# Kernel tuning notes

Hardware: AMD Instinct MI355X
Metric: run time of the kernel (lower is better)

The kernel has to match this reference:

```python
import jax, jax.numpy as jnp
import numpy as np

H, C, HID, L, NF, B = 4, 128, 128, 3, 5, 32  # heads, per-head dim, hidden, layers, node feats, graphs
LN_EPS = 1e-5


def setup_inputs() -> dict:
    key = jax.random.key(0)
    ks = jax.random.split(key, 12)
    N, E = 10000, 160000
    x = jax.random.normal(ks[0], (N, NF), dtype=jnp.float32)
    edge_index = jax.random.randint(ks[1], (2, E), 0, N, dtype=jnp.int64)
    batch = jnp.sort(jax.random.randint(ks[2], (N,), 0, B, dtype=jnp.int64))
    s = 0.1
    return {
        "x": x,
        "edge_index": edge_index,
        "batch": batch,
        "node_W": jax.random.normal(ks[3], (NF, HID), dtype=jnp.float32) * s,
        "node_b": jnp.zeros((HID,), dtype=jnp.float32),
        "Ws": jax.random.normal(ks[4], (L, HID, H * C), dtype=jnp.float32) * s,
        "att_srcs": jax.random.normal(ks[5], (L, H, C), dtype=jnp.float32) * s,
        "att_dsts": jax.random.normal(ks[6], (L, H, C), dtype=jnp.float32) * s,
        "biases": jnp.zeros((L, HID), dtype=jnp.float32),
        "ln_gs": jnp.ones((L, HID), dtype=jnp.float32),
        "ln_bs": jnp.zeros((L, HID), dtype=jnp.float32),
    }


def _layer_norm(x, g, b):
    mu = jnp.mean(x, axis=-1, keepdims=True)
    var = jnp.mean(jnp.square(x - mu), axis=-1, keepdims=True)
    return (x - mu) * jax.lax.rsqrt(var + LN_EPS) * g + b


def _gat_layer(x, W, att_src, att_dst, bias, src, dst, N):
    # x: [N, HID]; PyG GATConv, heads=H, concat=False (mean over heads)
    h = (x @ W).reshape(N, H, C)                       # [N,H,C]
    a_src = jnp.sum(h * att_src, axis=-1)              # [N,H]
    a_dst = jnp.sum(h * att_dst, axis=-1)              # [N,H]
    e = jax.nn.leaky_relu(a_src[src] + a_dst[dst], 0.2)  # [E,H]
    # edge-softmax over destination neighborhoods (numerically stable)
    m = jax.ops.segment_max(e, dst, num_segments=N)
    ex = jnp.exp(e - m[dst])
    denom = jax.ops.segment_sum(ex, dst, num_segments=N)
    alpha = ex / (denom[dst] + 1e-16)                  # [E,H]
    msg = h[src] * alpha[:, :, None]                   # [E,H,C]
    out = jax.ops.segment_sum(msg, dst, num_segments=N)  # [N,H,C]
    return out.mean(axis=1) + bias                     # concat=False -> head mean


def reference(x, edge_index, batch, node_W, node_b, Ws, att_srcs, att_dsts,
              biases, ln_gs, ln_bs):
    N = x.shape[0]
    loop = jnp.arange(N, dtype=edge_index.dtype)
    src = jnp.concatenate([edge_index[0], loop])       # PyG adds self-loops
    dst = jnp.concatenate([edge_index[1], loop])

    h = jax.nn.relu(x @ node_W + node_b)               # [N,HID]
    for l in range(L):
        h_new = _gat_layer(h, Ws[l], att_srcs[l], att_dsts[l], biases[l], src, dst, N)
        h_new = _layer_norm(h_new, ln_gs[l], ln_bs[l])
        h = jax.nn.relu(h_new) + h                     # residual; dropout is identity in eval

    # global mean pool over graphs
    sums = jax.ops.segment_sum(h, batch, num_segments=B)
    cnts = jax.ops.segment_sum(jnp.ones((N, 1), h.dtype), batch, num_segments=B)
    graph_emb = sums / jnp.maximum(cnts, 1.0)
    return h, graph_emb
```

## Files before the change

kernel.cpp:

```cpp
#include <hip/hip_runtime.h>
#include <math.h>

#define N_NODES 10000
#define N_EDGES 160000
#define E2 (N_EDGES + N_NODES)
#define HIDDEN 128
#define NHEAD 4
#define NB 32
#define LN_EPS 1e-5f

#define T_INPUT (N_NODES * HIDDEN)
#define T_HIST  (T_INPUT + N_EDGES)
#define T_CONV  (T_HIST + 3 * 512 * 128)
#define T_BOUND (T_CONV + N_NODES)
#define T_TOTAL T_BOUND

typedef __attribute__((ext_vector_type(8))) short bf16x8;
typedef __attribute__((ext_vector_type(4))) float f32x4;

__device__ __forceinline__ unsigned short f2bf(float f) {
    unsigned int u = __float_as_uint(f);
    u += 0x7fffu + ((u >> 16) & 1u);
    return (unsigned short)(u >> 16);
}
__device__ __forceinline__ float bf2f_lo(unsigned int u) { return __uint_as_float(u << 16); }
__device__ __forceinline__ float bf2f_hi(unsigned int u) { return __uint_as_float(u & 0xffff0000u); }

__global__ __launch_bounds__(256) void k_pre(const float* __restrict__ x,
                                             const float* __restrict__ W,
                                             const float* __restrict__ b,
                                             const int* __restrict__ ei,
                                             const int* __restrict__ batch,
                                             const float* __restrict__ Ws,
                                             float* __restrict__ h,
                                             unsigned short* __restrict__ hb,
                                             int* counts, int* gstart, int* gend,
                                             unsigned short* __restrict__ Btb) {
    int t = blockIdx.x * blockDim.x + threadIdx.x;
    if (t < T_INPUT) {
        int n = t >> 7, c = t & 127;
        float s = b[c];
        #pragma unroll
        for (int k = 0; k < 5; k++) s += x[n * 5 + k] * W[k * HIDDEN + c];
        float r = fmaxf(s, 0.f);
        h[t] = r;
        hb[t] = f2bf(r);
    } else if (t < T_HIST) {
        int e = t - T_INPUT;
        atomicAdd(&counts[ei[N_EDGES + e]], 1);
    } else if (t < T_CONV) {
        int i = t - T_HIST;
        int l = i >> 16, rem = i & 65535;
        int n = rem >> 7, k = rem & 127;
        Btb[i] = f2bf(Ws[l * 65536 + k * 512 + n]);
    } else if (t < T_BOUND) {
        int n = t - T_CONV;
        int bb = batch[n];
        if (n == 0 || batch[n - 1] != bb) gstart[bb] = n;
        if (n == N_NODES - 1 || batch[n + 1] != bb) gend[bb] = n + 1;
    }
}

__global__ void k_scan(const int* __restrict__ counts, int* rowptr, int* cursor) {
    __shared__ int sums[1024];
    int t = threadIdx.x;
    const int per = 10;
    int base = t * per;
    int loc[per];
    int s = 0;
    for (int i = 0; i < per; i++) {
        int idx = base + i;
        int v = (idx < N_NODES) ? counts[idx] + 1 : 0;
        loc[i] = s; s += v;
    }
    sums[t] = s;
    __syncthreads();
    for (int off = 1; off < 1024; off <<= 1) {
        int v = (t >= off) ? sums[t - off] : 0;
        __syncthreads();
        sums[t] += v;
        __syncthreads();
    }
    int prefix = (t > 0) ? sums[t - 1] : 0;
    for (int i = 0; i < per; i++) {
        int idx = base + i;
        if (idx < N_NODES) { int r = prefix + loc[i]; rowptr[idx] = r; cursor[idx] = r; }
    }
    if (t == 1023) rowptr[N_NODES] = sums[1023];
}

template <int SCATTER>
__global__ __launch_bounds__(256) void k_gemm_att(const unsigned short* __restrict__ Ab,
                                                  const unsigned short* __restrict__ Bt,
                                                  const float* __restrict__ ws,
                                                  const float* __restrict__ wd,
                                                  unsigned short* __restrict__ Cb,
                                                  float* __restrict__ a_src,
                                                  float* __restrict__ a_dst,
                                                  const int* __restrict__ ei,
                                                  int* __restrict__ cursor,
                                                  int* __restrict__ csr_src) {
    if (SCATTER) {
        int e = (blockIdx.y * gridDim.x + blockIdx.x) * 256 + threadIdx.x;
        if (e < N_EDGES) {
            int s = ei[e], d = ei[N_EDGES + e];
            int pos = atomicAdd(&cursor[d], 1);
            csr_src[pos] = s;
        } else if (e < E2) {
            int n = e - N_EDGES;
            int pos = atomicAdd(&cursor[n], 1);
            csr_src[pos] = n;
        }
    }
    int wave = threadIdx.x >> 6, lane = threadIdx.x & 63;
    int q = lane >> 4, u = lane & 15;
    int h = blockIdx.x;
    int rowgrp = wave & 1, colhalf = wave >> 1;
    int mbase = blockIdx.y * 32 + rowgrp * 16;
    int colbase = h * 128 + colhalf * 64;
    int arow = mbase + u;
    if (arow > N_NODES - 1) arow = N_NODES - 1;
    bf16x8 a[4];
    #pragma unroll
    for (int k0 = 0; k0 < 4; k0++)
        a[k0] = *(const bf16x8*)(Ab + (size_t)arow * 128 + k0 * 32 + q * 8);
    f32x4 acc[4];
    #pragma unroll
    for (int nb = 0; nb < 4; nb++) acc[nb] = (f32x4){0.f, 0.f, 0.f, 0.f};
    #pragma unroll
    for (int nb = 0; nb < 4; nb++) {
        const unsigned short* bp = Bt + (size_t)(colbase + nb * 16 + u) * 128 + q * 8;
        #pragma unroll
        for (int k0 = 0; k0 < 4; k0++) {
            bf16x8 bfr = *(const bf16x8*)(bp + k0 * 32);
            acc[nb] = __builtin_amdgcn_mfma_f32_16x16x32_bf16(a[k0], bfr, acc[nb], 0, 0, 0);
        }
    }
    #pragma unroll
    for (int nb = 0; nb < 4; nb++) {
        int col = colbase + nb * 16 + u;
        #pragma unroll
        for (int r = 0; r < 4; r++) {
            int row = mbase + q * 4 + r;
            if (row < N_NODES) Cb[(size_t)row * 512 + col] = f2bf(acc[nb][r]);
        }
    }
    float ps[4] = {}, pd[4] = {};
    #pragma unroll
    for (int nb = 0; nb < 4; nb++) {
        int cl = colhalf * 64 + nb * 16 + u;
        float wsv = ws[h * 128 + cl], wdv = wd[h * 128 + cl];
        #pragma unroll
        for (int r = 0; r < 4; r++) { ps[r] += acc[nb][r] * wsv; pd[r] += acc[nb][r] * wdv; }
    }
    #pragma unroll
    for (int d = 1; d < 16; d <<= 1) {
        #pragma unroll
        for (int r = 0; r < 4; r++) {
            ps[r] += __shfl_xor(ps[r], d);
            pd[r] += __shfl_xor(pd[r], d);
        }
    }
    __shared__ float ls[2][2][16], ldd[2][2][16];
    if (u == 0) {
        #pragma unroll
        for (int r = 0; r < 4; r++) {
            ls[rowgrp][colhalf][q * 4 + r] = ps[r];
            ldd[rowgrp][colhalf][q * 4 + r] = pd[r];
        }
    }
    __syncthreads();
    if (colhalf == 0 && lane < 16) {
        int row = mbase + lane;
        if (row < N_NODES) {
            a_src[row * 4 + h] = ls[rowgrp][0][lane] + ls[rowgrp][1][lane];
            a_dst[row * 4 + h] = ldd[rowgrp][0][lane] + ldd[rowgrp][1][lane];
        }
    }
}

__global__ __launch_bounds__(256) void k_agg(const uint4* __restrict__ hb4,
                                             const int* __restrict__ rowptr,
                                             const int* __restrict__ csr,
                                             const float* __restrict__ a_src,
                                             const float* __restrict__ a_dst,
                                             const float* __restrict__ bias,
                                             const float* __restrict__ lng,
                                             const float* __restrict__ lnb,
                                             float* __restrict__ h,
                                             unsigned short* __restrict__ hbn) {
    int wave = threadIdx.x >> 6;
    int lane = threadIdx.x & 63;
    int n = blockIdx.x * 4 + wave;
    if (n >= N_NODES) return;
    int hl = lane >> 4;
    int pos = lane & 15;
    int off = rowptr[n];
    int deg = rowptr[n + 1] - off;
    float adn = a_dst[n * 4 + hl];
    float mA = -INFINITY, dA = 0.f;
    float mB = -INFINITY, dB = 0.f;
    float oA[8] = {}, oB[8] = {};
    for (int base = 0; base < deg; base += 64) {
        int cnt = min(64, deg - base);
        int s = (lane < cnt) ? csr[off + base + lane] : 0;
        int i1 = (1 < cnt) ? 1 : 0;
        int s0 = __shfl(s, 0), s1 = __shfl(s, i1);
        uint4 u0 = hb4[(size_t)s0 * 64 + lane];
        float av0 = a_src[s0 * 4 + hl];
        uint4 u1 = hb4[(size_t)s1 * 64 + lane];
        float av1 = a_src[s1 * 4 + hl];
        for (int i = 0; i < cnt; i += 2) {
            int j2 = (i + 2 < cnt) ? i + 2 : cnt - 1;
            int j3 = (i + 3 < cnt) ? i + 3 : cnt - 1;
            int s2 = __shfl(s, j2), s3 = __shfl(s, j3);
            uint4 u2 = hb4[(size_t)s2 * 64 + lane];
            float av2 = a_src[s2 * 4 + hl];
            uint4 u3 = hb4[(size_t)s3 * 64 + lane];
            float av3 = a_src[s3 * 4 + hl];
            {
                float t = av0 + adn;
                float e = t > 0.f ? t : 0.2f * t;
                float nm = fmaxf(mA, e);
                float sc = __expf(mA - nm);
                float p = __expf(e - nm);
                dA = dA * sc + p;
                oA[0] = oA[0] * sc + p * bf2f_lo(u0.x);
                oA[1] = oA[1] * sc + p * bf2f_hi(u0.x);
                oA[2] = oA[2] * sc + p * bf2f_lo(u0.y);
                oA[3] = oA[3] * sc + p * bf2f_hi(u0.y);
                oA[4] = oA[4] * sc + p * bf2f_lo(u0.z);
                oA[5] = oA[5] * sc + p * bf2f_hi(u0.z);
                oA[6] = oA[6] * sc + p * bf2f_lo(u0.w);
                oA[7] = oA[7] * sc + p * bf2f_hi(u0.w);
                mA = nm;
            }
            if (i + 1 < cnt) {
                float t = av1 + adn;
                float e = t > 0.f ? t : 0.2f * t;
                float nm = fmaxf(mB, e);
                float sc = __expf(mB - nm);
                float p = __expf(e - nm);
                dB = dB * sc + p;
                oB[0] = oB[0] * sc + p * bf2f_lo(u1.x);
                oB[1] = oB[1] * sc + p * bf2f_hi(u1.x);
                oB[2] = oB[2] * sc + p * bf2f_lo(u1.y);
                oB[3] = oB[3] * sc + p * bf2f_hi(u1.y);
                oB[4] = oB[4] * sc + p * bf2f_lo(u1.z);
                oB[5] = oB[5] * sc + p * bf2f_hi(u1.z);
                oB[6] = oB[6] * sc + p * bf2f_lo(u1.w);
                oB[7] = oB[7] * sc + p * bf2f_hi(u1.w);
                mB = nm;
            }
            u0 = u2; av0 = av2;
            u1 = u3; av1 = av3;
        }
    }
    float M = fmaxf(mA, mB);
    float sA = __expf(mA - M);
    float sB = (mB == -INFINITY) ? 0.f : __expf(mB - M);
    float denom = dA * sA + dB * sB;
    float o[8];
    #pragma unroll
    for (int k = 0; k < 8; k++) o[k] = oA[k] * sA + oB[k] * sB;

    float inv = 1.f / (denom + 1e-16f);
    #pragma unroll
    for (int k = 0; k < 8; k++) o[k] *= inv;
    #pragma unroll
    for (int k = 0; k < 8; k++) {
        o[k] += __shfl_xor(o[k], 16);
        o[k] += __shfl_xor(o[k], 32);
    }
    float v[8], sv = 0.f, sq = 0.f;
    #pragma unroll
    for (int k = 0; k < 8; k++) {
        float b = bias[8 * pos + k];
        v[k] = 0.25f * o[k] + b;
        sv += v[k]; sq += v[k] * v[k];
    }
    #pragma unroll
    for (int d = 8; d > 0; d >>= 1) {
        sv += __shfl_xor(sv, d);
        sq += __shfl_xor(sq, d);
    }
    float mu = sv * (1.f / 128.f);
    float var = sq * (1.f / 128.f) - mu * mu;
    float rs = rsqrtf(var + LN_EPS);
    if (hl == 0) {
        float* hrow = h + (size_t)n * 128 + 8 * pos;
        float4 old0 = *(const float4*)(hrow);
        float4 old1 = *(const float4*)(hrow + 4);
        float r[8];
        #pragma unroll
        for (int k = 0; k < 8; k++) {
            float y = (v[k] - mu) * rs * lng[8 * pos + k] + lnb[8 * pos + k];
            r[k] = fmaxf(y, 0.f);
        }
        float w[8] = {r[0] + old0.x, r[1] + old0.y, r[2] + old0.z, r[3] + old0.w,
                      r[4] + old1.x, r[5] + old1.y, r[6] + old1.z, r[7] + old1.w};
        *(float4*)(hrow) = make_float4(w[0], w[1], w[2], w[3]);
        *(float4*)(hrow + 4) = make_float4(w[4], w[5], w[6], w[7]);
        ushort4 p0, p1;
        p0.x = f2bf(w[0]); p0.y = f2bf(w[1]); p0.z = f2bf(w[2]); p0.w = f2bf(w[3]);
        p1.x = f2bf(w[4]); p1.y = f2bf(w[5]); p1.z = f2bf(w[6]); p1.w = f2bf(w[7]);
        unsigned short* hbrow = hbn + (size_t)n * 128 + 8 * pos;
        *(ushort4*)(hbrow) = p0;
        *(ushort4*)(hbrow + 4) = p1;
    }
}

#define POOL_CHUNK 32
__global__ __launch_bounds__(128) void k_pool_sum(const float* __restrict__ h,
                                                  const int* __restrict__ batch,
                                                  const int* __restrict__ gstart,
                                                  const int* __restrict__ gend,
                                                  float* __restrict__ gout) {
    int n0 = blockIdx.x * POOL_CHUNK;
    int c = threadIdx.x;
    int nend = min(n0 + POOL_CHUNK, N_NODES);
    if (n0 >= N_NODES) return;
    int cur = batch[n0];
    float acc = 0.f;
    for (int n = n0; n < nend; n++) {
        int b = batch[n];
        if (b != cur) {
            float inv = 1.f / (float)max(gend[cur] - gstart[cur], 1);
            atomicAdd(&gout[cur * HIDDEN + c], acc * inv);
            acc = 0.f; cur = b;
        }
        acc += h[(size_t)n * HIDDEN + c];
    }
    float inv = 1.f / (float)max(gend[cur] - gstart[cur], 1);
    atomicAdd(&gout[cur * HIDDEN + c], acc * inv);
}

extern "C" void kernel_launch(void* const* d_in, const int* in_sizes, int n_in,
                              void* d_out, int out_size, void* d_ws, size_t ws_size,
                              hipStream_t stream) {
    const float* x      = (const float*)d_in[0];
    const int*   ei     = (const int*)d_in[1];
    const int*   batch  = (const int*)d_in[2];
    const float* node_W = (const float*)d_in[3];
    const float* node_b = (const float*)d_in[4];
    const float* Ws     = (const float*)d_in[5];
    const float* att_s  = (const float*)d_in[6];
    const float* att_d  = (const float*)d_in[7];
    const float* biases = (const float*)d_in[8];
    const float* ln_g   = (const float*)d_in[9];
    const float* ln_b   = (const float*)d_in[10];

    float* out = (float*)d_out;
    float* h = out;
    float* gout = out + (size_t)N_NODES * HIDDEN;

    char* w = (char*)d_ws;
    auto carve = [&](size_t bytes) {
        void* p = (void*)w;
        w += (bytes + 255) & ~(size_t)255;
        return p;
    };
    int* rowptr  = (int*)carve((N_NODES + 1) * sizeof(int));
    int* cursor  = (int*)carve(N_NODES * sizeof(int));
    int* counts  = (int*)carve(N_NODES * sizeof(int));
    int* csr     = (int*)carve((E2 + 16) * sizeof(int));
    int* gstart  = (int*)carve(NB * sizeof(int));
    int* gend    = (int*)carve(NB * sizeof(int));
    float* a_src = (float*)carve((size_t)N_NODES * NHEAD * sizeof(float));
    float* a_dst = (float*)carve((size_t)N_NODES * NHEAD * sizeof(float));
    unsigned short* hb  = (unsigned short*)carve((size_t)N_NODES * 512 * sizeof(unsigned short));
    unsigned short* hbx = (unsigned short*)carve((size_t)N_NODES * HIDDEN * sizeof(unsigned short));
    unsigned short* Btb = (unsigned short*)carve((size_t)3 * 512 * 128 * sizeof(unsigned short));

    hipMemsetAsync(counts, 0, N_NODES * sizeof(int), stream);
    hipMemsetAsync(gout, 0, NB * HIDDEN * sizeof(float), stream);

    k_pre<<<(T_TOTAL + 255) / 256, 256, 0, stream>>>(x, node_W, node_b, ei, batch, Ws,
                                                     h, hbx, counts, gstart, gend, Btb);
    k_scan<<<1, 1024, 0, stream>>>(counts, rowptr, cursor);

    for (int l = 0; l < 3; l++) {
        if (l == 0) {
            k_gemm_att<1><<<dim3(4, (N_NODES + 31) / 32), 256, 0, stream>>>(
                hbx, Btb + (size_t)l * 512 * 128,
                att_s + l * NHEAD * 128, att_d + l * NHEAD * 128,
                hb, a_src, a_dst, ei, cursor, csr);
        } else {
            k_gemm_att<0><<<dim3(4, (N_NODES + 31) / 32), 256, 0, stream>>>(
                hbx, Btb + (size_t)l * 512 * 128,
                att_s + l * NHEAD * 128, att_d + l * NHEAD * 128,
                hb, a_src, a_dst, ei, cursor, csr);
        }
        k_agg<<<(N_NODES + 3) / 4, 256, 0, stream>>>((const uint4*)hb, rowptr, csr,
                                           a_src, a_dst,
                                           biases + l * HIDDEN, ln_g + l * HIDDEN,
                                           ln_b + l * HIDDEN, h, hbx);
    }
    k_pool_sum<<<(N_NODES + POOL_CHUNK - 1) / POOL_CHUNK, 128, 0, stream>>>(
        h, batch, gstart, gend, gout);
}
```

Baseline: 260.0 us.

## Move degree histogram into single-block scan and replace atomic pooling with per-graph blocks

The in-degree histogram moves out of the wide preprocessing kernel and into the single-block scan kernel, which counts with LDS atomics over 160k edges. This drops the counts buffer and its memset. The global mean pool becomes one 512-thread block per graph that reduces rows in shared memory and writes results directly, which removes the gout memset and the global atomics. The risk is that one block now serially processes all 160k edges in the scan, which may cost more than the saved memsets and launches.

```diff
diff --git a/kernel.cpp b/kernel.cpp
--- a/kernel.cpp
+++ b/kernel.cpp
@@ -10,8 +10,7 @@
 #define LN_EPS 1e-5f
 
 #define T_INPUT (N_NODES * HIDDEN)
-#define T_HIST  (T_INPUT + N_EDGES)
-#define T_CONV  (T_HIST + 3 * 512 * 128)
+#define T_CONV  (T_INPUT + 3 * 512 * 128)
 #define T_BOUND (T_CONV + N_NODES)
 #define T_TOTAL T_BOUND
 
@@ -29,12 +28,11 @@
 __global__ __launch_bounds__(256) void k_pre(const float* __restrict__ x,
                                              const float* __restrict__ W,
                                              const float* __restrict__ b,
-                                             const int* __restrict__ ei,
                                              const int* __restrict__ batch,
                                              const float* __restrict__ Ws,
                                              float* __restrict__ h,
                                              unsigned short* __restrict__ hb,
-                                             int* counts, int* gstart, int* gend,
+                                             int* gstart, int* gend,
                                              unsigned short* __restrict__ Btb) {
     int t = blockIdx.x * blockDim.x + threadIdx.x;
     if (t < T_INPUT) {
@@ -45,11 +43,8 @@
         float r = fmaxf(s, 0.f);
         h[t] = r;
         hb[t] = f2bf(r);
-    } else if (t < T_HIST) {
-        int e = t - T_INPUT;
-        atomicAdd(&counts[ei[N_EDGES + e]], 1);
     } else if (t < T_CONV) {
-        int i = t - T_HIST;
+        int i = t - T_INPUT;
         int l = i >> 16, rem = i & 65535;
         int n = rem >> 7, k = rem & 127;
         Btb[i] = f2bf(Ws[l * 65536 + k * 512 + n]);
@@ -61,16 +56,24 @@
     }
 }
 
-__global__ void k_scan(const int* __restrict__ counts, int* rowptr, int* cursor) {
+__global__ __launch_bounds__(1024) void k_scan(const int* __restrict__ ei,
+                                               int* rowptr, int* cursor) {
+    __shared__ int cnt[N_NODES];
     __shared__ int sums[1024];
     int t = threadIdx.x;
+    for (int i = t; i < N_NODES; i += 1024) cnt[i] = 0;
+    __syncthreads();
+    for (int e = t; e < N_EDGES; e += 1024)
+        atomicAdd(&cnt[ei[N_EDGES + e]], 1);
+    __syncthreads();
     const int per = 10;
     int base = t * per;
     int loc[per];
     int s = 0;
+    #pragma unroll
     for (int i = 0; i < per; i++) {
         int idx = base + i;
-        int v = (idx < N_NODES) ? counts[idx] + 1 : 0;
+        int v = (idx < N_NODES) ? cnt[idx] + 1 : 0;
         loc[i] = s; s += v;
     }
     sums[t] = s;
@@ -82,6 +85,7 @@
         __syncthreads();
     }
     int prefix = (t > 0) ? sums[t - 1] : 0;
+    #pragma unroll
     for (int i = 0; i < per; i++) {
         int idx = base + i;
         if (idx < N_NODES) { int r = prefix + loc[i]; rowptr[idx] = r; cursor[idx] = r; }
@@ -310,29 +314,24 @@
     }
 }
 
-#define POOL_CHUNK 32
-__global__ __launch_bounds__(128) void k_pool_sum(const float* __restrict__ h,
-                                                  const int* __restrict__ batch,
-                                                  const int* __restrict__ gstart,
-                                                  const int* __restrict__ gend,
-                                                  float* __restrict__ gout) {
-    int n0 = blockIdx.x * POOL_CHUNK;
-    int c = threadIdx.x;
-    int nend = min(n0 + POOL_CHUNK, N_NODES);
-    if (n0 >= N_NODES) return;
-    int cur = batch[n0];
+__global__ __launch_bounds__(512) void k_pool(const float* __restrict__ h,
+                                              const int* __restrict__ gstart,
+                                              const int* __restrict__ gend,
+                                              float* __restrict__ gout) {
+    __shared__ float sm[4][128];
+    int g = blockIdx.x;
+    int c = threadIdx.x & 127;
+    int r = threadIdx.x >> 7;
+    int s = gstart[g], e = gend[g];
     float acc = 0.f;
-    for (int n = n0; n < nend; n++) {
-        int b = batch[n];
-        if (b != cur) {
-            float inv = 1.f / (float)max(gend[cur] - gstart[cur], 1);
-            atomicAdd(&gout[cur * HIDDEN + c], acc * inv);
-            acc = 0.f; cur = b;
-        }
-        acc += h[(size_t)n * HIDDEN + c];
-    }
-    float inv = 1.f / (float)max(gend[cur] - gstart[cur], 1);
-    atomicAdd(&gout[cur * HIDDEN + c], acc * inv);
+    for (int n = s + r; n < e; n += 4)
+        acc += h[(size_t)n * 128 + c];
+    sm[r][c] = acc;
+    __syncthreads();
+    if (r == 0) {
+        float tot = sm[0][c] + sm[1][c] + sm[2][c] + sm[3][c];
+        gout[g * 128 + c] = tot / (float)max(e - s, 1);
+    }
 }
 
 extern "C" void kernel_launch(void* const* d_in, const int* in_sizes, int n_in,
@@ -362,7 +361,6 @@
     };
     int* rowptr  = (int*)carve((N_NODES + 1) * sizeof(int));
     int* cursor  = (int*)carve(N_NODES * sizeof(int));
-    int* counts  = (int*)carve(N_NODES * sizeof(int));
     int* csr     = (int*)carve((E2 + 16) * sizeof(int));
     int* gstart  = (int*)carve(NB * sizeof(int));
     int* gend    = (int*)carve(NB * sizeof(int));
@@ -372,12 +370,9 @@
     unsigned short* hbx = (unsigned short*)carve((size_t)N_NODES * HIDDEN * sizeof(unsigned short));
     unsigned short* Btb = (unsigned short*)carve((size_t)3 * 512 * 128 * sizeof(unsigned short));
 
-    hipMemsetAsync(counts, 0, N_NODES * sizeof(int), stream);
-    hipMemsetAsync(gout, 0, NB * HIDDEN * sizeof(float), stream);
-
-    k_pre<<<(T_TOTAL + 255) / 256, 256, 0, stream>>>(x, node_W, node_b, ei, batch, Ws,
-                                                     h, hbx, counts, gstart, gend, Btb);
-    k_scan<<<1, 1024, 0, stream>>>(counts, rowptr, cursor);
+    k_pre<<<(T_TOTAL + 255) / 256, 256, 0, stream>>>(x, node_W, node_b, batch, Ws,
+                                                     h, hbx, gstart, gend, Btb);
+    k_scan<<<1, 1024, 0, stream>>>(ei, rowptr, cursor);
 
     for (int l = 0; l < 3; l++) {
         if (l == 0) {
@@ -396,6 +391,5 @@
                                            biases + l * HIDDEN, ln_g + l * HIDDEN,
                                            ln_b + l * HIDDEN, h, hbx);
     }
-    k_pool_sum<<<(N_NODES + POOL_CHUNK - 1) / POOL_CHUNK, 128, 0, stream>>>(
-        h, batch, gstart, gend, gout);
-}
+    k_pool<<<NB, 512, 0, stream>>>(h, gstart, gend, gout);
+}
```

After: 305.9 us. 17.7% more time.
